# Optimization experiments

Hardware: AMD Instinct MI355X
Metric: run time of the kernel (lower is better)

Reference implementation:

```python
import jax, jax.numpy as jnp
from jax import lax
import numpy as np

D_MODEL = 1024
D_STATE = 64
D_CONV = 4
EXPAND = 2
HEADDIM = 64
D_INNER = EXPAND * D_MODEL          # 2048
NHEADS = D_INNER // HEADDIM         # 32
CHUNK = 64
CONV_DIM = D_INNER + 2 * D_STATE    # 2176
D_IN_PROJ = 2 * D_INNER + 2 * D_STATE + NHEADS  # 4256
B_SZ = 4
SEQLEN = 2048
EPS = 1e-5


def _silu(x):
    return x * jax.nn.sigmoid(x)


def _segsum(x):
    # x: [..., T]; returns [..., T, T] with [i,j] = sum_{j<k<=i} x[k], -inf above diag
    T = x.shape[-1]
    xe = jnp.broadcast_to(x[..., None], x.shape + (T,))
    strict_lower = jnp.tril(jnp.ones((T, T), bool), -1)
    xe = jnp.where(strict_lower, xe, 0.0)
    s = jnp.cumsum(xe, axis=-2)
    lower = jnp.tril(jnp.ones((T, T), bool), 0)
    return jnp.where(lower, s, -jnp.inf)


def setup_inputs() -> dict:
    key = jax.random.key(0)
    ks = jax.random.split(key, 5)
    u = jax.random.normal(ks[0], (B_SZ, SEQLEN, D_MODEL), jnp.float32)
    W_in = jax.random.normal(ks[1], (D_IN_PROJ, D_MODEL), jnp.float32) * 0.02
    conv_w = jax.random.normal(ks[2], (CONV_DIM, 1, D_CONV), jnp.float32) * 0.2  # depthwise kernel
    conv_b = jnp.zeros((CONV_DIM,), jnp.float32)
    dt_bias = jax.random.uniform(ks[3], (NHEADS,), jnp.float32, -1.0, 1.0)
    A_log = jnp.log(jnp.linspace(1.0, float(NHEADS), NHEADS)).astype(jnp.float32)
    D = jnp.ones((NHEADS,), jnp.float32)
    norm_w = jnp.ones((D_INNER,), jnp.float32)
    W_out = jax.random.normal(ks[4], (D_MODEL, D_INNER), jnp.float32) * 0.02
    return dict(u=u, W_in=W_in, conv_w=conv_w, conv_b=conv_b, dt_bias=dt_bias,
                A_log=A_log, D=D, norm_w=norm_w, W_out=W_out)


def reference(u, W_in, conv_w, conv_b, dt_bias, A_log, D, norm_w, W_out):
    b, s, _ = u.shape
    A = -jnp.exp(A_log)                                   # [H]
    zxbcdt = u @ W_in.T                                   # [b,s,D_IN_PROJ]
    z = zxbcdt[..., :D_INNER]
    xBC = zxbcdt[..., D_INNER:D_INNER + CONV_DIM]
    dt = jax.nn.softplus(zxbcdt[..., D_INNER + CONV_DIM:] + dt_bias)  # [b,s,H]

    # causal depthwise conv1d (left pad d_conv-1 == torch pad-both + slice[:s])
    xc = lax.conv_general_dilated(
        xBC.transpose(0, 2, 1), conv_w, window_strides=(1,),
        padding=[(D_CONV - 1, 0)], feature_group_count=CONV_DIM,
        dimension_numbers=('NCH', 'OIH', 'NCH'))
    xBC = _silu(xc.transpose(0, 2, 1) + conv_b)           # [b,s,CONV_DIM]

    x = xBC[..., :D_INNER].reshape(b, s, NHEADS, HEADDIM)
    Bm = xBC[..., D_INNER:D_INNER + D_STATE]              # [b,s,N]
    Cm = xBC[..., D_INNER + D_STATE:]                     # [b,s,N]

    # SSD chunked scan
    nch = s // CHUNK
    xs = (x * dt[..., None]).reshape(b, nch, CHUNK, NHEADS, HEADDIM)
    Ad = (A * dt).reshape(b, nch, CHUNK, NHEADS)
    Br = Bm.reshape(b, nch, CHUNK, D_STATE)
    Cr = Cm.reshape(b, nch, CHUNK, D_STATE)
    A_ch = Ad.transpose(0, 1, 3, 2)                       # [b,c,h,l]
    A_cum = jnp.cumsum(A_ch, axis=-1)
    L = jnp.exp(_segsum(A_ch))                            # [b,c,h,l,l]
    Y_diag = jnp.einsum('bcln,bcsn,bchls,bcshp->bclhp', Cr, Br, L, xs)
    decay_states = jnp.exp(A_cum[..., -1:] - A_cum)       # [b,c,h,l]
    states = jnp.einsum('bchl,bcln,bclhp->bchpn', decay_states, Br, xs)
    init = jnp.zeros((b, 1, NHEADS, HEADDIM, D_STATE), xs.dtype)
    states = jnp.concatenate([init, states], axis=1)      # [b,c+1,h,p,n]
    total_decay = jnp.pad(A_cum[..., -1].transpose(0, 2, 1), ((0, 0), (0, 0), (1, 0)))
    decay_chunk = jnp.exp(_segsum(total_decay))           # [b,h,c+1,c+1]
    new_states = jnp.einsum('bhzc,bchpn->bzhpn', decay_chunk, states)
    states = new_states[:, :-1]                           # [b,c,h,p,n]
    state_decay_out = jnp.exp(A_cum)
    Y_off = jnp.einsum('bcln,bchpn,bchl->bclhp', Cr, states, state_decay_out)
    y = (Y_diag + Y_off).reshape(b, s, NHEADS, HEADDIM)

    y = y + x * D[:, None]
    y = y.reshape(b, s, D_INNER)
    # gated RMSNorm
    y = y * _silu(z)
    y = y * lax.rsqrt(jnp.mean(y * y, axis=-1, keepdims=True) + EPS) * norm_w
    return y @ W_out.T
```

## Files before the change

kernel.cpp:

```cpp
#include <hip/hip_runtime.h>
#include <hip/hip_bf16.h>

#define BSZ 4
#define SEQ 2048
#define DMODEL 1024
#define DINNER 2048
#define DSTATE 64
#define NH 32
#define HD 64
#define CKL 64
#define NCH 32
#define CONVD 2176
#define DPROJ 4256
#define N1 4224
#define MTOT 8192
#define YSTR 72

typedef __hip_bfloat16 bf16;
typedef __attribute__((ext_vector_type(8))) short short8;
typedef __attribute__((ext_vector_type(4))) short short4_;
typedef __attribute__((ext_vector_type(2))) short short2_;
typedef __attribute__((ext_vector_type(4))) float f32x4;

__device__ __forceinline__ float sigmoidf_(float x) { return 1.0f / (1.0f + __expf(-x)); }
__device__ __forceinline__ float bits2f(short s) { return __uint_as_float(((unsigned)(unsigned short)s) << 16); }
__device__ __forceinline__ short f2bits(float f) {
    bf16 h = __float2bfloat16(f);
    return *reinterpret_cast<short*>(&h);
}

__device__ __forceinline__ void gl_lds16(const bf16* g, bf16* l) {
    __builtin_amdgcn_global_load_lds((const __attribute__((address_space(1))) void*)g,
                                     (__attribute__((address_space(3))) void*)l, 16, 0, 0);
}

__device__ __forceinline__ void store_val(float* p, float v) { *p = v; }
__device__ __forceinline__ void store_val(bf16* p, float v) { *p = __float2bfloat16(v); }

__global__ void k_cvt(const float* __restrict__ src, bf16* __restrict__ dst, int n) {
    int i = blockIdx.x * 256 + threadIdx.x;
    int g = i * 4;
    if (g < n) {
        f32x4 f = *(const f32x4*)&src[g];
        short4_ o;
#pragma unroll
        for (int j = 0; j < 4; j++) o[j] = f2bits(f[j]);
        *(short4_*)&dst[g] = o;
    }
}

template <typename TOUT>
__global__ __launch_bounds__(256) void k_gemm_bt(const bf16* __restrict__ A, const bf16* __restrict__ W,
                                                 TOUT* __restrict__ C, int N, int K) {
    __shared__ __align__(16) bf16 lA[128 * 64];
    __shared__ __align__(16) bf16 lB[128 * 64];
    const int tid = threadIdx.x;
    const int lane = tid & 63, w = tid >> 6;
    const int wm = w >> 1, wn = w & 1;
    const int lr = lane & 15, lk = lane >> 4;
    const int m0 = blockIdx.y * 128, n0 = blockIdx.x * 128;

    f32x4 acc[4][4];
#pragma unroll
    for (int i = 0; i < 4; i++)
#pragma unroll
        for (int j = 0; j < 4; j++) acc[i][j] = (f32x4){0.f, 0.f, 0.f, 0.f};

    const int r = tid >> 3;
    const int cs = ((tid & 7) ^ (r & 7)) * 8;
    const bf16* ga = A + (size_t)(m0 + r) * K + cs;
    const bf16* gb = W + (size_t)(n0 + r) * K + cs;
    bf16* la0 = lA + tid * 8;
    bf16* lb0 = lB + tid * 8;
    const int sx = (lr & 7);

    for (int kt = 0; kt < K; kt += 64) {
#pragma unroll
        for (int i = 0; i < 4; i++) {
            gl_lds16(ga + kt + (size_t)(32 * i) * K, la0 + 2048 * i);
            gl_lds16(gb + kt + (size_t)(32 * i) * K, lb0 + 2048 * i);
        }
        __syncthreads();
#pragma unroll
        for (int hh = 0; hh < 2; hh++) {
            const int cb = ((lk + 4 * hh) ^ sx) * 8;
            short8 af[4], bfr[4];
#pragma unroll
            for (int im = 0; im < 4; im++)
                af[im] = *(const short8*)&lA[(wm * 64 + im * 16 + lr) * 64 + cb];
#pragma unroll
            for (int jn = 0; jn < 4; jn++)
                bfr[jn] = *(const short8*)&lB[(wn * 64 + jn * 16 + lr) * 64 + cb];
#pragma unroll
            for (int im = 0; im < 4; im++)
#pragma unroll
                for (int jn = 0; jn < 4; jn++)
                    acc[im][jn] = __builtin_amdgcn_mfma_f32_16x16x32_bf16(af[im], bfr[jn], acc[im][jn], 0, 0, 0);
        }
        __syncthreads();
    }
#pragma unroll
    for (int im = 0; im < 4; im++) {
        int row = m0 + wm * 64 + im * 16 + lk * 4;
#pragma unroll
        for (int jn = 0; jn < 4; jn++) {
            int col = n0 + wn * 64 + jn * 16 + lr;
            TOUT* cp = C + (size_t)row * N + col;
#pragma unroll
            for (int rr = 0; rr < 4; rr++) store_val(cp + (size_t)rr * N, acc[im][jn][rr]);
        }
    }
}

__global__ __launch_bounds__(256) void k_prep(const float* __restrict__ u, const float* __restrict__ W_in,
                                              const float* __restrict__ dt_bias,
                                              bf16* __restrict__ u_b, float* __restrict__ dtb) {
    __shared__ __align__(16) float us[8 * DMODEL];
    const int t0 = blockIdx.x * 8;
    const int tid = threadIdx.x;
    const float* ur = u + (size_t)t0 * DMODEL;
    bf16* ub = u_b + (size_t)t0 * DMODEL;
#pragma unroll
    for (int i = 0; i < 8; i++) {
        int idx = (i * 256 + tid) * 4;
        f32x4 v = *(const f32x4*)&ur[idx];
        *(f32x4*)&us[idx] = v;
        short4_ o;
#pragma unroll
        for (int j = 0; j < 4; j++) o[j] = f2bits(v[j]);
        *(short4_*)&ub[idx] = o;
    }
    __syncthreads();
    const int h = tid >> 3, sub = tid & 7;
    const float* wr = W_in + (size_t)(DPROJ - NH + h) * DMODEL;
    float s[8] = {};
    for (int k = sub * 4; k < DMODEL; k += 32) {
        f32x4 w4 = *(const f32x4*)&wr[k];
#pragma unroll
        for (int rr = 0; rr < 8; rr++) {
            const float* up = &us[rr * DMODEL + k];
            s[rr] += up[0] * w4[0] + up[1] * w4[1] + up[2] * w4[2] + up[3] * w4[3];
        }
    }
#pragma unroll
    for (int rr = 0; rr < 8; rr++) {
        s[rr] += __shfl_down(s[rr], 4, 8);
        s[rr] += __shfl_down(s[rr], 2, 8);
        s[rr] += __shfl_down(s[rr], 1, 8);
    }
    if (sub == 0) {
        float bh = dt_bias[h];
#pragma unroll
        for (int rr = 0; rr < 8; rr++) {
            float x = s[rr] + bh;
            dtb[(size_t)(t0 + rr) * NH + h] = (x > 20.f) ? x : log1pf(__expf(x));
        }
    }
}

__global__ void k_conv(const bf16* __restrict__ zx, const float* __restrict__ cw,
                       const float* __restrict__ cb, bf16* __restrict__ xbc) {
    int i = blockIdx.x * 256 + threadIdx.x;
    int g = i * 4;
    if (g >= MTOT * CONVD) return;
    int c0 = g % CONVD;
    int t = g / CONVD;
    int s = t & (SEQ - 1);
    const short* base = (const short*)(zx + (size_t)t * N1 + DINNER + c0);
    f32x4 w0 = *(const f32x4*)&cw[(c0 + 0) * 4];
    f32x4 w1 = *(const f32x4*)&cw[(c0 + 1) * 4];
    f32x4 w2 = *(const f32x4*)&cw[(c0 + 2) * 4];
    f32x4 w3 = *(const f32x4*)&cw[(c0 + 3) * 4];
    f32x4 a = *(const f32x4*)&cb[c0];
#pragma unroll
    for (int k = 0; k < 4; k++) {
        int st = s - 3 + k;
        if (st >= 0) {
            short4_ v = *(const short4_*)(base + (long)(k - 3) * N1);
            a[0] += bits2f(v[0]) * w0[k];
            a[1] += bits2f(v[1]) * w1[k];
            a[2] += bits2f(v[2]) * w2[k];
            a[3] += bits2f(v[3]) * w3[k];
        }
    }
    short4_ o;
#pragma unroll
    for (int j = 0; j < 4; j++) o[j] = f2bits(a[j] * sigmoidf_(a[j]));
    *(short4_*)&xbc[g] = o;
}

__global__ __launch_bounds__(256) void k_cstate(const bf16* __restrict__ xbc, const float* __restrict__ dt,
                                                const float* __restrict__ A_log, bf16* __restrict__ states,
                                                float* __restrict__ totdec) {
    __shared__ __align__(16) short Bt[CKL * YSTR];
    __shared__ __align__(16) short Xt[CKL * YSTR];
    __shared__ float sf[CKL];
    const int h = blockIdx.x, c = blockIdx.y, b = blockIdx.z;
    const int tid = threadIdx.x;
    const int row0 = b * SEQ + c * CKL;
    const float Ah = -__expf(A_log[h]);

    if (tid < 64) {
        float dv = dt[(size_t)(row0 + tid) * NH + h];
        float v = Ah * dv;
#pragma unroll
        for (int d = 1; d < 64; d <<= 1) {
            float o = __shfl_up(v, d);
            if (tid >= d) v += o;
        }
        float tot = __shfl(v, 63);
        sf[tid] = __expf(tot - v) * dv;
        if (tid == 63) totdec[(b * NCH + c) * NH + h] = tot;
    }
    {
        const int n0 = (tid & 15) * 4;
#pragma unroll
        for (int it = 0; it < 4; it++) {
            int l = it * 16 + (tid >> 4);
            const short* rp = (const short*)(xbc + (size_t)(row0 + l) * CONVD);
            short4_ b4 = *(const short4_*)&rp[DINNER + n0];
            short4_ x4 = *(const short4_*)&rp[h * HD + n0];
#pragma unroll
            for (int j = 0; j < 4; j++) {
                Bt[(n0 + j) * YSTR + l] = b4[j];
                Xt[(n0 + j) * YSTR + l] = x4[j];
            }
        }
    }
    __syncthreads();
    {
        const int l0 = (tid & 15) * 4;
        f32x4 f = *(const f32x4*)&sf[l0];
#pragma unroll
        for (int it = 0; it < 4; it++) {
            int n = it * 16 + (tid >> 4);
            short* p = &Bt[n * YSTR + l0];
            short4_ v = *(short4_*)p;
#pragma unroll
            for (int j = 0; j < 4; j++) v[j] = f2bits(bits2f(v[j]) * f[j]);
            *(short4_*)p = v;
        }
    }
    __syncthreads();
    const int lane = tid & 63, w = tid >> 6;
    const int lr = lane & 15, lk = lane >> 4;
    short8 af0 = *(const short8*)&Xt[(16 * w + lr) * YSTR + lk * 8];
    short8 af1 = *(const short8*)&Xt[(16 * w + lr) * YSTR + 32 + lk * 8];
    f32x4 acc[4];
#pragma unroll
    for (int t = 0; t < 4; t++) {
        short8 b0 = *(const short8*)&Bt[(16 * t + lr) * YSTR + lk * 8];
        short8 b1 = *(const short8*)&Bt[(16 * t + lr) * YSTR + 32 + lk * 8];
        acc[t] = __builtin_amdgcn_mfma_f32_16x16x32_bf16(af0, b0, (f32x4){0.f, 0.f, 0.f, 0.f}, 0, 0, 0);
        acc[t] = __builtin_amdgcn_mfma_f32_16x16x32_bf16(af1, b1, acc[t], 0, 0, 0);
    }
    __syncthreads();
    short* Ys = Bt;
#pragma unroll
    for (int t = 0; t < 4; t++) {
        int n = 16 * t + lr;
#pragma unroll
        for (int rr = 0; rr < 4; rr++)
            Ys[(16 * w + lk * 4 + rr) * YSTR + n] = f2bits(acc[t][rr]);
    }
    short* sp = (short*)(states + (((size_t)(b * NCH + c) * NH + h) << 12));
    {
        int p = 16 * w + (lane >> 2);
        int n0 = (lane & 3) * 16;
        short8 a0 = *(const short8*)&Ys[p * YSTR + n0];
        short8 a1 = *(const short8*)&Ys[p * YSTR + n0 + 8];
        *(short8*)&sp[p * 64 + n0] = a0;
        *(short8*)&sp[p * 64 + n0 + 8] = a1;
    }
}

__global__ void k_scan(bf16* __restrict__ states, const float* __restrict__ totdec) {
    int i = blockIdx.x * 256 + threadIdx.x;
    if (i >= BSZ * NH * 2048) return;
    int pn = (i & 2047) * 2;
    int h = (i >> 11) & 31;
    int b = i >> 16;
    float s0 = 0.f, s1 = 0.f;
    size_t strideC = (size_t)NH << 12;
    size_t off = (((size_t)(b * NCH) * NH + h) << 12) + pn;
    const float* tdp = totdec + (b * NCH) * NH + h;
    for (int c = 0; c < NCH; c++) {
        short2_ v = *(short2_*)&states[off];
        short2_ o; o[0] = f2bits(s0); o[1] = f2bits(s1);
        *(short2_*)&states[off] = o;
        float e = __expf(tdp[c * NH]);
        s0 = s0 * e + bits2f(v[0]);
        s1 = s1 * e + bits2f(v[1]);
        off += strideC;
    }
}

__global__ __launch_bounds__(256) void k_y(const bf16* __restrict__ xbc, const float* __restrict__ dt,
                                           const float* __restrict__ A_log, const float* __restrict__ Dp,
                                           const bf16* __restrict__ states, bf16* __restrict__ zx) {
    __shared__ __align__(16) short Cs[CKL * YSTR];
    __shared__ __align__(16) short Bs[CKL * YSTR];
    __shared__ __align__(16) short Ss[CKL * YSTR];
    __shared__ __align__(16) short Xt[CKL * YSTR];
    __shared__ __align__(16) short Gs[4 * 16 * YSTR];
    __shared__ float sdt[CKL], sAc[CKL];
    const int h = blockIdx.x, c = blockIdx.y, b = blockIdx.z;
    const int tid = threadIdx.x;
    const int row0 = b * SEQ + c * CKL;
    const float Ah = -__expf(A_log[h]);
    const float Dh = Dp[h];

    if (tid < 64) {
        float dv = dt[(size_t)(row0 + tid) * NH + h];
        sdt[tid] = dv;
        float v = Ah * dv;
#pragma unroll
        for (int d = 1; d < 64; d <<= 1) {
            float o = __shfl_up(v, d);
            if (tid >= d) v += o;
        }
        sAc[tid] = v;
    }
    const short* spg = (const short*)(states + (((size_t)(b * NCH + c) * NH + h) << 12));
    {
        const int n0 = (tid & 15) * 4;
#pragma unroll
        for (int it = 0; it < 4; it++) {
            int l = it * 16 + (tid >> 4);
            const short* rp = (const short*)(xbc + (size_t)(row0 + l) * CONVD);
            *(short4_*)&Cs[l * YSTR + n0] = *(const short4_*)&rp[DINNER + DSTATE + n0];
            *(short4_*)&Bs[l * YSTR + n0] = *(const short4_*)&rp[DINNER + n0];
            *(short4_*)&Ss[l * YSTR + n0] = *(const short4_*)&spg[l * 64 + n0];
            short4_ x4 = *(const short4_*)&rp[h * HD + n0];
#pragma unroll
            for (int j = 0; j < 4; j++) Xt[(n0 + j) * YSTR + l] = x4[j];
        }
    }
    __syncthreads();

    const int lane = tid & 63, w = tid >> 6;
    const int lr = lane & 15, lk = lane >> 4;
    short* gw = Gs + w * 16 * YSTR;

    short8 cf0 = *(const short8*)&Cs[(16 * w + lr) * YSTR + lk * 8];
    short8 cf1 = *(const short8*)&Cs[(16 * w + lr) * YSTR + 32 + lk * 8];

    f32x4 acc[4];
#pragma unroll
    for (int t = 0; t < 4; t++) {
        short8 s0 = *(const short8*)&Ss[(16 * t + lr) * YSTR + lk * 8];
        short8 s1 = *(const short8*)&Ss[(16 * t + lr) * YSTR + 32 + lk * 8];
        acc[t] = __builtin_amdgcn_mfma_f32_16x16x32_bf16(cf0, s0, (f32x4){0.f, 0.f, 0.f, 0.f}, 0, 0, 0);
        acc[t] = __builtin_amdgcn_mfma_f32_16x16x32_bf16(cf1, s1, acc[t], 0, 0, 0);
    }
    float sAcl[4], el[4];
#pragma unroll
    for (int rr = 0; rr < 4; rr++) {
        sAcl[rr] = sAc[16 * w + lk * 4 + rr];
        el[rr] = __expf(sAcl[rr]);
    }
#pragma unroll
    for (int t = 0; t < 4; t++)
#pragma unroll
        for (int rr = 0; rr < 4; rr++) acc[t][rr] *= el[rr];

#pragma unroll
    for (int t = 0; t < 4; t++) {
        short8 b0 = *(const short8*)&Bs[(16 * t + lr) * YSTR + lk * 8];
        short8 b1 = *(const short8*)&Bs[(16 * t + lr) * YSTR + 32 + lk * 8];
        f32x4 g = __builtin_amdgcn_mfma_f32_16x16x32_bf16(cf0, b0, (f32x4){0.f, 0.f, 0.f, 0.f}, 0, 0, 0);
        g = __builtin_amdgcn_mfma_f32_16x16x32_bf16(cf1, b1, g, 0, 0, 0);
        int s = 16 * t + lr;
        float sAcs = sAc[s], dts = sdt[s];
#pragma unroll
        for (int rr = 0; rr < 4; rr++) {
            int l = 16 * w + lk * 4 + rr;
            float v = (s <= l) ? g[rr] * __expf(sAcl[rr] - sAcs) * dts : 0.f;
            gw[(lk * 4 + rr) * YSTR + s] = f2bits(v);
        }
    }
    short8 gf0 = *(const short8*)&gw[lr * YSTR + lk * 8];
    short8 gf1 = *(const short8*)&gw[lr * YSTR + 32 + lk * 8];
#pragma unroll
    for (int t = 0; t < 4; t++) {
        short8 x0 = *(const short8*)&Xt[(16 * t + lr) * YSTR + lk * 8];
        short8 x1 = *(const short8*)&Xt[(16 * t + lr) * YSTR + 32 + lk * 8];
        acc[t] = __builtin_amdgcn_mfma_f32_16x16x32_bf16(gf0, x0, acc[t], 0, 0, 0);
        acc[t] = __builtin_amdgcn_mfma_f32_16x16x32_bf16(gf1, x1, acc[t], 0, 0, 0);
    }
    __syncthreads();
    short* Ys = Cs;
#pragma unroll
    for (int t = 0; t < 4; t++) {
        int p = 16 * t + lr;
#pragma unroll
        for (int rr = 0; rr < 4; rr++) {
            int l = 16 * w + lk * 4 + rr;
            float y = acc[t][rr] + Dh * bits2f(Xt[p * YSTR + l]);
            Ys[l * YSTR + p] = f2bits(y);
        }
    }
    {
        int l = 16 * w + (lane >> 2);
        int p0 = (lane & 3) * 16;
        short8 y0 = *(const short8*)&Ys[l * YSTR + p0];
        short8 y1 = *(const short8*)&Ys[l * YSTR + p0 + 8];
        short* zp = (short*)(zx + (size_t)(row0 + l) * N1 + h * HD + p0);
        short8 z0 = *(const short8*)zp;
        short8 z1 = *(const short8*)(zp + 8);
        short8 o0, o1;
#pragma unroll
        for (int j = 0; j < 8; j++) {
            float z = bits2f(z0[j]);
            o0[j] = f2bits(bits2f(y0[j]) * (z * sigmoidf_(z)));
        }
#pragma unroll
        for (int j = 0; j < 8; j++) {
            float z = bits2f(z1[j]);
            o1[j] = f2bits(bits2f(y1[j]) * (z * sigmoidf_(z)));
        }
        *(short8*)zp = o0;
        *(short8*)(zp + 8) = o1;
    }
}

__global__ __launch_bounds__(256) void k_norm(const bf16* __restrict__ zx, const float* __restrict__ nw,
                                              bf16* __restrict__ yb) {
    __shared__ float red[4];
    int t = blockIdx.x, tid = threadIdx.x;
    const short* row = (const short*)(zx + (size_t)t * N1);
    short8 v8 = *(const short8*)&row[tid * 8];
    float v[8];
    float ss = 0.f;
#pragma unroll
    for (int i = 0; i < 8; i++) {
        v[i] = bits2f(v8[i]);
        ss += v[i] * v[i];
    }
#pragma unroll
    for (int d = 32; d > 0; d >>= 1) ss += __shfl_down(ss, d);
    if ((tid & 63) == 0) red[tid >> 6] = ss;
    __syncthreads();
    float scale = rsqrtf((red[0] + red[1] + red[2] + red[3]) * (1.0f / DINNER) + 1e-5f);
    f32x4 w0 = *(const f32x4*)&nw[tid * 8];
    f32x4 w1 = *(const f32x4*)&nw[tid * 8 + 4];
    short8 o;
#pragma unroll
    for (int i = 0; i < 4; i++) o[i] = f2bits(v[i] * scale * w0[i]);
#pragma unroll
    for (int i = 0; i < 4; i++) o[4 + i] = f2bits(v[4 + i] * scale * w1[i]);
    *(short8*)&((short*)yb)[(size_t)t * DINNER + tid * 8] = o;
}

extern "C" void kernel_launch(void* const* d_in, const int* in_sizes, int n_in,
                              void* d_out, int out_size, void* d_ws, size_t ws_size,
                              hipStream_t stream) {
    const float* u       = (const float*)d_in[0];
    const float* W_in    = (const float*)d_in[1];
    const float* conv_w  = (const float*)d_in[2];
    const float* conv_b  = (const float*)d_in[3];
    const float* dt_bias = (const float*)d_in[4];
    const float* A_log   = (const float*)d_in[5];
    const float* Dp      = (const float*)d_in[6];
    const float* norm_w  = (const float*)d_in[7];
    const float* W_out   = (const float*)d_in[8];
    float* out = (float*)d_out;

    char* ws = (char*)d_ws;
    bf16* zx     = (bf16*)ws;  ws += (size_t)MTOT * N1 * 2;
    bf16* xbc    = (bf16*)ws;  ws += (size_t)MTOT * CONVD * 2;
    bf16* wout_b = (bf16*)ws;  ws += (size_t)DMODEL * DINNER * 2;
    float* dtb   = (float*)ws; ws += (size_t)MTOT * NH * 4;
    float* td    = (float*)ws; ws += (size_t)BSZ * NCH * NH * 4;
    bf16* y_b    = (bf16*)xbc;

    bf16* u_b   = (bf16*)d_out;
    bf16* win_b = (bf16*)((char*)d_out + (size_t)MTOT * DMODEL * 2);
    bf16* st    = (bf16*)d_out;

    k_prep<<<MTOT / 8, 256, 0, stream>>>(u, W_in, dt_bias, u_b, dtb);
    k_cvt<<<(N1 * DMODEL / 4 + 255) / 256, 256, 0, stream>>>(W_in, win_b, N1 * DMODEL);
    k_cvt<<<(DMODEL * DINNER / 4 + 255) / 256, 256, 0, stream>>>(W_out, wout_b, DMODEL * DINNER);

    k_gemm_bt<bf16><<<dim3(N1 / 128, MTOT / 128), 256, 0, stream>>>(u_b, win_b, zx, N1, DMODEL);

    k_conv<<<(MTOT * CONVD / 4 + 255) / 256, 256, 0, stream>>>(zx, conv_w, conv_b, xbc);

    k_cstate<<<dim3(NH, NCH, BSZ), 256, 0, stream>>>(xbc, dtb, A_log, st, td);
    k_scan<<<(BSZ * NH * 2048 + 255) / 256, 256, 0, stream>>>(st, td);
    k_y<<<dim3(NH, NCH, BSZ), 256, 0, stream>>>(xbc, dtb, A_log, Dp, st, zx);

    k_norm<<<MTOT, 256, 0, stream>>>(zx, norm_w, y_b);

    k_gemm_bt<float><<<dim3(DMODEL / 128, MTOT / 128), 256, 0, stream>>>(y_b, wout_b, out, DMODEL, DINNER);
}
```

Measured before the change: 400.7 us.

## Fuse chunk-state, scan and output SSD kernels into one sequential-chunk kernel

Replaces the three SSD kernels (per-chunk state, inter-chunk scan, per-chunk output) with a single kernel. Each block owns one batch, one head and half of the head dimension, and walks all chunks in order, carrying the running state in shared memory as fp32. The next chunk's inputs are prefetched into registers while the current chunk is computed. The dt buffer is also transposed to head-major so each block reads it contiguously. This removes the global round trip of the bf16 states and two launches, but drops to 256 blocks that each run a serial 32-step loop with two barriers per step, which may leave latency exposed.

```diff
diff --git a/kernel.cpp b/kernel.cpp
--- a/kernel.cpp
+++ b/kernel.cpp
@@ -19,7 +19,6 @@
 typedef __hip_bfloat16 bf16;
 typedef __attribute__((ext_vector_type(8))) short short8;
 typedef __attribute__((ext_vector_type(4))) short short4_;
-typedef __attribute__((ext_vector_type(2))) short short2_;
 typedef __attribute__((ext_vector_type(4))) float f32x4;
 
 __device__ __forceinline__ float sigmoidf_(float x) { return 1.0f / (1.0f + __expf(-x)); }
@@ -114,7 +113,7 @@
 
 __global__ __launch_bounds__(256) void k_prep(const float* __restrict__ u, const float* __restrict__ W_in,
                                               const float* __restrict__ dt_bias,
-                                              bf16* __restrict__ u_b, float* __restrict__ dtb) {
+                                              bf16* __restrict__ u_b, float* __restrict__ dtt) {
     __shared__ __align__(16) float us[8 * DMODEL];
     const int t0 = blockIdx.x * 8;
     const int tid = threadIdx.x;
@@ -153,7 +152,7 @@
 #pragma unroll
         for (int rr = 0; rr < 8; rr++) {
             float x = s[rr] + bh;
-            dtb[(size_t)(t0 + rr) * NH + h] = (x > 20.f) ? x : log1pf(__expf(x));
+            dtt[(size_t)h * MTOT + t0 + rr] = (x > 20.f) ? x : log1pf(__expf(x));
         }
     }
 }
@@ -189,238 +188,183 @@
     *(short4_*)&xbc[g] = o;
 }
 
-__global__ __launch_bounds__(256) void k_cstate(const bf16* __restrict__ xbc, const float* __restrict__ dt,
-                                                const float* __restrict__ A_log, bf16* __restrict__ states,
-                                                float* __restrict__ totdec) {
-    __shared__ __align__(16) short Bt[CKL * YSTR];
-    __shared__ __align__(16) short Xt[CKL * YSTR];
-    __shared__ float sf[CKL];
-    const int h = blockIdx.x, c = blockIdx.y, b = blockIdx.z;
+__global__ __launch_bounds__(256) void k_ssd(const bf16* __restrict__ xbc, const float* __restrict__ dtt,
+                                             const float* __restrict__ A_log, const float* __restrict__ Dp,
+                                             bf16* __restrict__ zx) {
+    __shared__ __align__(16) short Ct[64 * YSTR];
+    __shared__ __align__(16) short Bt[64 * YSTR];
+    __shared__ __align__(16) short Bn[64 * YSTR];
+    __shared__ __align__(16) short Xt[32 * YSTR];
+    __shared__ __align__(16) short Xd[32 * YSTR];
+    __shared__ __align__(16) short Sb[32 * YSTR];
+    __shared__ __align__(16) short Gs[4 * 16 * YSTR];
+    __shared__ __align__(16) float Sf[32 * 68];
+    __shared__ float sdt2[2][64], sAc2[2][64], sf2[2][64], set2[2];
+
+    const int ph = blockIdx.x, h = blockIdx.y, b = blockIdx.z;
     const int tid = threadIdx.x;
-    const int row0 = b * SEQ + c * CKL;
-    const float Ah = -__expf(A_log[h]);
-
-    if (tid < 64) {
-        float dv = dt[(size_t)(row0 + tid) * NH + h];
-        float v = Ah * dv;
-#pragma unroll
-        for (int d = 1; d < 64; d <<= 1) {
-            float o = __shfl_up(v, d);
-            if (tid >= d) v += o;
-        }
-        float tot = __shfl(v, 63);
-        sf[tid] = __expf(tot - v) * dv;
-        if (tid == 63) totdec[(b * NCH + c) * NH + h] = tot;
-    }
-    {
-        const int n0 = (tid & 15) * 4;
-#pragma unroll
-        for (int it = 0; it < 4; it++) {
-            int l = it * 16 + (tid >> 4);
-            const short* rp = (const short*)(xbc + (size_t)(row0 + l) * CONVD);
-            short4_ b4 = *(const short4_*)&rp[DINNER + n0];
-            short4_ x4 = *(const short4_*)&rp[h * HD + n0];
-#pragma unroll
-            for (int j = 0; j < 4; j++) {
-                Bt[(n0 + j) * YSTR + l] = b4[j];
-                Xt[(n0 + j) * YSTR + l] = x4[j];
-            }
-        }
-    }
-    __syncthreads();
-    {
-        const int l0 = (tid & 15) * 4;
-        f32x4 f = *(const f32x4*)&sf[l0];
-#pragma unroll
-        for (int it = 0; it < 4; it++) {
-            int n = it * 16 + (tid >> 4);
-            short* p = &Bt[n * YSTR + l0];
-            short4_ v = *(short4_*)p;
-#pragma unroll
-            for (int j = 0; j < 4; j++) v[j] = f2bits(bits2f(v[j]) * f[j]);
-            *(short4_*)p = v;
-        }
-    }
-    __syncthreads();
     const int lane = tid & 63, w = tid >> 6;
     const int lr = lane & 15, lk = lane >> 4;
-    short8 af0 = *(const short8*)&Xt[(16 * w + lr) * YSTR + lk * 8];
-    short8 af1 = *(const short8*)&Xt[(16 * w + lr) * YSTR + 32 + lk * 8];
-    f32x4 acc[4];
-#pragma unroll
-    for (int t = 0; t < 4; t++) {
-        short8 b0 = *(const short8*)&Bt[(16 * t + lr) * YSTR + lk * 8];
-        short8 b1 = *(const short8*)&Bt[(16 * t + lr) * YSTR + 32 + lk * 8];
-        acc[t] = __builtin_amdgcn_mfma_f32_16x16x32_bf16(af0, b0, (f32x4){0.f, 0.f, 0.f, 0.f}, 0, 0, 0);
-        acc[t] = __builtin_amdgcn_mfma_f32_16x16x32_bf16(af1, b1, acc[t], 0, 0, 0);
-    }
-    __syncthreads();
-    short* Ys = Bt;
-#pragma unroll
-    for (int t = 0; t < 4; t++) {
-        int n = 16 * t + lr;
-#pragma unroll
-        for (int rr = 0; rr < 4; rr++)
-            Ys[(16 * w + lk * 4 + rr) * YSTR + n] = f2bits(acc[t][rr]);
-    }
-    short* sp = (short*)(states + (((size_t)(b * NCH + c) * NH + h) << 12));
-    {
-        int p = 16 * w + (lane >> 2);
-        int n0 = (lane & 3) * 16;
-        short8 a0 = *(const short8*)&Ys[p * YSTR + n0];
-        short8 a1 = *(const short8*)&Ys[p * YSTR + n0 + 8];
-        *(short8*)&sp[p * 64 + n0] = a0;
-        *(short8*)&sp[p * 64 + n0 + 8] = a1;
-    }
-}
-
-__global__ void k_scan(bf16* __restrict__ states, const float* __restrict__ totdec) {
-    int i = blockIdx.x * 256 + threadIdx.x;
-    if (i >= BSZ * NH * 2048) return;
-    int pn = (i & 2047) * 2;
-    int h = (i >> 11) & 31;
-    int b = i >> 16;
-    float s0 = 0.f, s1 = 0.f;
-    size_t strideC = (size_t)NH << 12;
-    size_t off = (((size_t)(b * NCH) * NH + h) << 12) + pn;
-    const float* tdp = totdec + (b * NCH) * NH + h;
-    for (int c = 0; c < NCH; c++) {
-        short2_ v = *(short2_*)&states[off];
-        short2_ o; o[0] = f2bits(s0); o[1] = f2bits(s1);
-        *(short2_*)&states[off] = o;
-        float e = __expf(tdp[c * NH]);
-        s0 = s0 * e + bits2f(v[0]);
-        s1 = s1 * e + bits2f(v[1]);
-        off += strideC;
-    }
-}
-
-__global__ __launch_bounds__(256) void k_y(const bf16* __restrict__ xbc, const float* __restrict__ dt,
-                                           const float* __restrict__ A_log, const float* __restrict__ Dp,
-                                           const bf16* __restrict__ states, bf16* __restrict__ zx) {
-    __shared__ __align__(16) short Cs[CKL * YSTR];
-    __shared__ __align__(16) short Bs[CKL * YSTR];
-    __shared__ __align__(16) short Ss[CKL * YSTR];
-    __shared__ __align__(16) short Xt[CKL * YSTR];
-    __shared__ __align__(16) short Gs[4 * 16 * YSTR];
-    __shared__ float sdt[CKL], sAc[CKL];
-    const int h = blockIdx.x, c = blockIdx.y, b = blockIdx.z;
-    const int tid = threadIdx.x;
-    const int row0 = b * SEQ + c * CKL;
     const float Ah = -__expf(A_log[h]);
     const float Dh = Dp[h];
-
+    const int xcol = h * HD + ph * 32;
+
+    const int lrow = tid >> 2, c0 = (tid & 3) * 16, px = (tid & 3) * 8;
+    const int zl = 16 * w + (lane >> 2), zp = (lane & 3) * 8;
+
+    short8 rC0, rC1, rB0, rB1, rX, rZ;
+    float rdt;
+    auto load_chunk = [&](int cc) {
+        int rows0 = b * SEQ + cc * CKL;
+        const short* rp = (const short*)(xbc + (size_t)(rows0 + lrow) * CONVD);
+        rC0 = *(const short8*)&rp[DINNER + DSTATE + c0];
+        rC1 = *(const short8*)&rp[DINNER + DSTATE + c0 + 8];
+        rB0 = *(const short8*)&rp[DINNER + c0];
+        rB1 = *(const short8*)&rp[DINNER + c0 + 8];
+        rX  = *(const short8*)&rp[xcol + px];
+        rZ  = *(const short8*)((const short*)zx + (size_t)(rows0 + zl) * N1 + xcol + zp);
+        rdt = dtt[(size_t)h * MTOT + rows0 + lane];
+    };
+
+    for (int i = tid; i < 32 * 68; i += 256) Sf[i] = 0.f;
+    load_chunk(0);
     if (tid < 64) {
-        float dv = dt[(size_t)(row0 + tid) * NH + h];
-        sdt[tid] = dv;
+        float dv = rdt;
         float v = Ah * dv;
 #pragma unroll
-        for (int d = 1; d < 64; d <<= 1) {
-            float o = __shfl_up(v, d);
-            if (tid >= d) v += o;
-        }
-        sAc[tid] = v;
-    }
-    const short* spg = (const short*)(states + (((size_t)(b * NCH + c) * NH + h) << 12));
-    {
-        const int n0 = (tid & 15) * 4;
-#pragma unroll
-        for (int it = 0; it < 4; it++) {
-            int l = it * 16 + (tid >> 4);
-            const short* rp = (const short*)(xbc + (size_t)(row0 + l) * CONVD);
-            *(short4_*)&Cs[l * YSTR + n0] = *(const short4_*)&rp[DINNER + DSTATE + n0];
-            *(short4_*)&Bs[l * YSTR + n0] = *(const short4_*)&rp[DINNER + n0];
-            *(short4_*)&Ss[l * YSTR + n0] = *(const short4_*)&spg[l * 64 + n0];
-            short4_ x4 = *(const short4_*)&rp[h * HD + n0];
-#pragma unroll
-            for (int j = 0; j < 4; j++) Xt[(n0 + j) * YSTR + l] = x4[j];
-        }
+        for (int d = 1; d < 64; d <<= 1) { float o = __shfl_up(v, d); if (tid >= d) v += o; }
+        float tot = __shfl(v, 63);
+        sdt2[0][tid] = dv; sAc2[0][tid] = v; sf2[0][tid] = __expf(tot - v) * dv;
+        if (tid == 63) set2[0] = __expf(tot);
     }
     __syncthreads();
 
-    const int lane = tid & 63, w = tid >> 6;
-    const int lr = lane & 15, lk = lane >> 4;
-    short* gw = Gs + w * 16 * YSTR;
-
-    short8 cf0 = *(const short8*)&Cs[(16 * w + lr) * YSTR + lk * 8];
-    short8 cf1 = *(const short8*)&Cs[(16 * w + lr) * YSTR + 32 + lk * 8];
-
-    f32x4 acc[4];
-#pragma unroll
-    for (int t = 0; t < 4; t++) {
-        short8 s0 = *(const short8*)&Ss[(16 * t + lr) * YSTR + lk * 8];
-        short8 s1 = *(const short8*)&Ss[(16 * t + lr) * YSTR + 32 + lk * 8];
-        acc[t] = __builtin_amdgcn_mfma_f32_16x16x32_bf16(cf0, s0, (f32x4){0.f, 0.f, 0.f, 0.f}, 0, 0, 0);
-        acc[t] = __builtin_amdgcn_mfma_f32_16x16x32_bf16(cf1, s1, acc[t], 0, 0, 0);
-    }
-    float sAcl[4], el[4];
-#pragma unroll
-    for (int rr = 0; rr < 4; rr++) {
-        sAcl[rr] = sAc[16 * w + lk * 4 + rr];
-        el[rr] = __expf(sAcl[rr]);
-    }
-#pragma unroll
-    for (int t = 0; t < 4; t++)
-#pragma unroll
-        for (int rr = 0; rr < 4; rr++) acc[t][rr] *= el[rr];
-
-#pragma unroll
-    for (int t = 0; t < 4; t++) {
-        short8 b0 = *(const short8*)&Bs[(16 * t + lr) * YSTR + lk * 8];
-        short8 b1 = *(const short8*)&Bs[(16 * t + lr) * YSTR + 32 + lk * 8];
-        f32x4 g = __builtin_amdgcn_mfma_f32_16x16x32_bf16(cf0, b0, (f32x4){0.f, 0.f, 0.f, 0.f}, 0, 0, 0);
-        g = __builtin_amdgcn_mfma_f32_16x16x32_bf16(cf1, b1, g, 0, 0, 0);
-        int s = 16 * t + lr;
-        float sAcs = sAc[s], dts = sdt[s];
-#pragma unroll
-        for (int rr = 0; rr < 4; rr++) {
-            int l = 16 * w + lk * 4 + rr;
-            float v = (s <= l) ? g[rr] * __expf(sAcl[rr] - sAcs) * dts : 0.f;
-            gw[(lk * 4 + rr) * YSTR + s] = f2bits(v);
-        }
-    }
-    short8 gf0 = *(const short8*)&gw[lr * YSTR + lk * 8];
-    short8 gf1 = *(const short8*)&gw[lr * YSTR + 32 + lk * 8];
-#pragma unroll
-    for (int t = 0; t < 4; t++) {
-        short8 x0 = *(const short8*)&Xt[(16 * t + lr) * YSTR + lk * 8];
-        short8 x1 = *(const short8*)&Xt[(16 * t + lr) * YSTR + 32 + lk * 8];
-        acc[t] = __builtin_amdgcn_mfma_f32_16x16x32_bf16(gf0, x0, acc[t], 0, 0, 0);
-        acc[t] = __builtin_amdgcn_mfma_f32_16x16x32_bf16(gf1, x1, acc[t], 0, 0, 0);
-    }
-    __syncthreads();
-    short* Ys = Cs;
-#pragma unroll
-    for (int t = 0; t < 4; t++) {
-        int p = 16 * t + lr;
-#pragma unroll
-        for (int rr = 0; rr < 4; rr++) {
-            int l = 16 * w + lk * 4 + rr;
-            float y = acc[t][rr] + Dh * bits2f(Xt[p * YSTR + l]);
-            Ys[l * YSTR + p] = f2bits(y);
-        }
-    }
-    {
-        int l = 16 * w + (lane >> 2);
-        int p0 = (lane & 3) * 16;
-        short8 y0 = *(const short8*)&Ys[l * YSTR + p0];
-        short8 y1 = *(const short8*)&Ys[l * YSTR + p0 + 8];
-        short* zp = (short*)(zx + (size_t)(row0 + l) * N1 + h * HD + p0);
-        short8 z0 = *(const short8*)zp;
-        short8 z1 = *(const short8*)(zp + 8);
-        short8 o0, o1;
+    for (int c = 0; c < NCH; c++) {
+        const int par = c & 1;
+        const int rows0 = b * SEQ + c * CKL;
+        *(short8*)&Ct[lrow * YSTR + c0] = rC0;
+        *(short8*)&Ct[lrow * YSTR + c0 + 8] = rC1;
+        *(short8*)&Bt[lrow * YSTR + c0] = rB0;
+        *(short8*)&Bt[lrow * YSTR + c0 + 8] = rB1;
 #pragma unroll
         for (int j = 0; j < 8; j++) {
-            float z = bits2f(z0[j]);
-            o0[j] = f2bits(bits2f(y0[j]) * (z * sigmoidf_(z)));
-        }
+            Bn[(c0 + j) * YSTR + lrow] = rB0[j];
+            Bn[(c0 + 8 + j) * YSTR + lrow] = rB1[j];
+        }
+        float sfl = sf2[par][lrow];
 #pragma unroll
         for (int j = 0; j < 8; j++) {
-            float z = bits2f(z1[j]);
-            o1[j] = f2bits(bits2f(y1[j]) * (z * sigmoidf_(z)));
-        }
-        *(short8*)zp = o0;
-        *(short8*)(zp + 8) = o1;
+            Xt[(px + j) * YSTR + lrow] = rX[j];
+            Xd[(px + j) * YSTR + lrow] = f2bits(bits2f(rX[j]) * sfl);
+        }
+        {
+            int sp = tid >> 3, sn = (tid & 7) * 8;
+            f32x4 a0 = *(const f32x4*)&Sf[sp * 68 + sn];
+            f32x4 a1 = *(const f32x4*)&Sf[sp * 68 + sn + 4];
+            short8 o;
+#pragma unroll
+            for (int j = 0; j < 4; j++) { o[j] = f2bits(a0[j]); o[4 + j] = f2bits(a1[j]); }
+            *(short8*)&Sb[sp * YSTR + sn] = o;
+        }
+        __syncthreads();
+
+        float etot = set2[par];
+        short8 zcur = rZ;
+        if (c + 1 < NCH) load_chunk(c + 1);
+
+        short8 cf0 = *(const short8*)&Ct[(16 * w + lr) * YSTR + lk * 8];
+        short8 cf1 = *(const short8*)&Ct[(16 * w + lr) * YSTR + 32 + lk * 8];
+        f32x4 acc[2];
+#pragma unroll
+        for (int t = 0; t < 2; t++) {
+            short8 s0 = *(const short8*)&Sb[(16 * t + lr) * YSTR + lk * 8];
+            short8 s1 = *(const short8*)&Sb[(16 * t + lr) * YSTR + 32 + lk * 8];
+            acc[t] = __builtin_amdgcn_mfma_f32_16x16x32_bf16(cf0, s0, (f32x4){0.f, 0.f, 0.f, 0.f}, 0, 0, 0);
+            acc[t] = __builtin_amdgcn_mfma_f32_16x16x32_bf16(cf1, s1, acc[t], 0, 0, 0);
+        }
+        float sAcl[4], el[4];
+#pragma unroll
+        for (int rr = 0; rr < 4; rr++) { sAcl[rr] = sAc2[par][16 * w + lk * 4 + rr]; el[rr] = __expf(sAcl[rr]); }
+#pragma unroll
+        for (int t = 0; t < 2; t++)
+#pragma unroll
+            for (int rr = 0; rr < 4; rr++) acc[t][rr] *= el[rr];
+        short* gw = Gs + w * 16 * YSTR;
+#pragma unroll
+        for (int t = 0; t < 4; t++) {
+            short8 b0 = *(const short8*)&Bt[(16 * t + lr) * YSTR + lk * 8];
+            short8 b1 = *(const short8*)&Bt[(16 * t + lr) * YSTR + 32 + lk * 8];
+            f32x4 g = __builtin_amdgcn_mfma_f32_16x16x32_bf16(cf0, b0, (f32x4){0.f, 0.f, 0.f, 0.f}, 0, 0, 0);
+            g = __builtin_amdgcn_mfma_f32_16x16x32_bf16(cf1, b1, g, 0, 0, 0);
+            int s = 16 * t + lr;
+            float sAcs = sAc2[par][s], dts = sdt2[par][s];
+#pragma unroll
+            for (int rr = 0; rr < 4; rr++) {
+                int l = 16 * w + lk * 4 + rr;
+                float v = (s <= l) ? g[rr] * __expf(sAcl[rr] - sAcs) * dts : 0.f;
+                gw[(lk * 4 + rr) * YSTR + s] = f2bits(v);
+            }
+        }
+        short8 gf0 = *(const short8*)&gw[lr * YSTR + lk * 8];
+        short8 gf1 = *(const short8*)&gw[lr * YSTR + 32 + lk * 8];
+#pragma unroll
+        for (int t = 0; t < 2; t++) {
+            short8 x0 = *(const short8*)&Xt[(16 * t + lr) * YSTR + lk * 8];
+            short8 x1 = *(const short8*)&Xt[(16 * t + lr) * YSTR + 32 + lk * 8];
+            acc[t] = __builtin_amdgcn_mfma_f32_16x16x32_bf16(gf0, x0, acc[t], 0, 0, 0);
+            acc[t] = __builtin_amdgcn_mfma_f32_16x16x32_bf16(gf1, x1, acc[t], 0, 0, 0);
+        }
+        {
+            int pw = w & 1, nh2 = w >> 1;
+            short8 xd0 = *(const short8*)&Xd[(16 * pw + lr) * YSTR + lk * 8];
+            short8 xd1 = *(const short8*)&Xd[(16 * pw + lr) * YSTR + 32 + lk * 8];
+#pragma unroll
+            for (int j = 0; j < 2; j++) {
+                int nt = 2 * nh2 + j;
+                short8 b0 = *(const short8*)&Bn[(16 * nt + lr) * YSTR + lk * 8];
+                short8 b1 = *(const short8*)&Bn[(16 * nt + lr) * YSTR + 32 + lk * 8];
+                f32x4 sacc = __builtin_amdgcn_mfma_f32_16x16x32_bf16(xd0, b0, (f32x4){0.f, 0.f, 0.f, 0.f}, 0, 0, 0);
+                sacc = __builtin_amdgcn_mfma_f32_16x16x32_bf16(xd1, b1, sacc, 0, 0, 0);
+#pragma unroll
+                for (int rr = 0; rr < 4; rr++) {
+                    int n = 16 * nt + lr;
+                    int p = 16 * pw + lk * 4 + rr;
+                    Sf[p * 68 + n] = Sf[p * 68 + n] * etot + sacc[rr];
+                }
+            }
+        }
+#pragma unroll
+        for (int t = 0; t < 2; t++) {
+#pragma unroll
+            for (int rr = 0; rr < 4; rr++) {
+                int p = 16 * t + lr;
+                int l = 16 * w + lk * 4 + rr;
+                float y = acc[t][rr] + Dh * bits2f(Xt[p * YSTR + l]);
+                Ct[l * YSTR + p] = f2bits(y);
+            }
+        }
+        {
+            short8 y8 = *(const short8*)&Ct[zl * YSTR + zp];
+            short* zpp = (short*)zx + (size_t)(rows0 + zl) * N1 + xcol + zp;
+            short8 o;
+#pragma unroll
+            for (int j = 0; j < 8; j++) {
+                float z = bits2f(zcur[j]);
+                o[j] = f2bits(bits2f(y8[j]) * (z * sigmoidf_(z)));
+            }
+            *(short8*)zpp = o;
+        }
+        if (c + 1 < NCH && tid < 64) {
+            int p2 = (c + 1) & 1;
+            float dv = rdt;
+            float v = Ah * dv;
+#pragma unroll
+            for (int d = 1; d < 64; d <<= 1) { float o = __shfl_up(v, d); if (tid >= d) v += o; }
+            float tot = __shfl(v, 63);
+            sdt2[p2][tid] = dv; sAc2[p2][tid] = v; sf2[p2][tid] = __expf(tot - v) * dv;
+            if (tid == 63) set2[p2] = __expf(tot);
+        }
+        __syncthreads();
     }
 }
 
@@ -470,15 +414,13 @@
     bf16* zx     = (bf16*)ws;  ws += (size_t)MTOT * N1 * 2;
     bf16* xbc    = (bf16*)ws;  ws += (size_t)MTOT * CONVD * 2;
     bf16* wout_b = (bf16*)ws;  ws += (size_t)DMODEL * DINNER * 2;
-    float* dtb   = (float*)ws; ws += (size_t)MTOT * NH * 4;
-    float* td    = (float*)ws; ws += (size_t)BSZ * NCH * NH * 4;
+    float* dtt   = (float*)ws; ws += (size_t)NH * MTOT * 4;
     bf16* y_b    = (bf16*)xbc;
 
     bf16* u_b   = (bf16*)d_out;
     bf16* win_b = (bf16*)((char*)d_out + (size_t)MTOT * DMODEL * 2);
-    bf16* st    = (bf16*)d_out;
-
-    k_prep<<<MTOT / 8, 256, 0, stream>>>(u, W_in, dt_bias, u_b, dtb);
+
+    k_prep<<<MTOT / 8, 256, 0, stream>>>(u, W_in, dt_bias, u_b, dtt);
     k_cvt<<<(N1 * DMODEL / 4 + 255) / 256, 256, 0, stream>>>(W_in, win_b, N1 * DMODEL);
     k_cvt<<<(DMODEL * DINNER / 4 + 255) / 256, 256, 0, stream>>>(W_out, wout_b, DMODEL * DINNER);
 
@@ -486,9 +428,7 @@
 
     k_conv<<<(MTOT * CONVD / 4 + 255) / 256, 256, 0, stream>>>(zx, conv_w, conv_b, xbc);
 
-    k_cstate<<<dim3(NH, NCH, BSZ), 256, 0, stream>>>(xbc, dtb, A_log, st, td);
-    k_scan<<<(BSZ * NH * 2048 + 255) / 256, 256, 0, stream>>>(st, td);
-    k_y<<<dim3(NH, NCH, BSZ), 256, 0, stream>>>(xbc, dtb, A_log, Dp, st, zx);
+    k_ssd<<<dim3(2, NH, BSZ), 256, 0, stream>>>(xbc, dtt, A_log, Dp, zx);
 
     k_norm<<<MTOT, 256, 0, stream>>>(zx, norm_w, y_b);
 
```

Result: no change. 401.9 us (+0.3%).
